# Kernel tuning notes

Hardware: AMD Instinct MI355X
Metric: run time of the kernel (lower is better)

## Reference

```python
import jax, jax.numpy as jnp
import numpy as np

KSIZE = 3
SCALE = 2


def setup_inputs() -> dict:
    key = jax.random.key(0)
    k1, k2, k3, k4 = jax.random.split(key, 4)
    B, C, H, W = 8, 3, 512, 512
    h, w = H // SCALE, W // SCALE
    return {
        "images": jax.random.uniform(k1, (B, C, H, W), jnp.float32),
        "kernels": jax.random.uniform(k2, (B, KSIZE ** 2, h, w), jnp.float32),
        "offsets_x": jax.random.uniform(k3, (B, KSIZE ** 2, h, w), jnp.float32),
        "offsets_y": jax.random.uniform(k4, (B, KSIZE ** 2, h, w), jnp.float32),
    }


def _softround(x, alpha=1.0):
    two_pi = 2.0 * jnp.pi
    return x - alpha * (jnp.sin(two_pi * x) / two_pi)


def _batch_bli(im, x, y):
    # im: [B, H, W, 3] channel-last; x, y: [B, N] float coords
    B, N = x.shape
    x0 = jnp.floor(x).astype(jnp.int32)
    x1 = x0 + 1
    y0 = jnp.floor(y).astype(jnp.int32)
    y1 = y0 + 1
    # original clamps x by im.shape[2] and y by im.shape[1] (square images)
    x0 = jnp.clip(x0, 0, im.shape[2] - 1)
    x1 = jnp.clip(x1, 0, im.shape[2] - 1)
    y0 = jnp.clip(y0, 0, im.shape[1] - 1)
    y1 = jnp.clip(y1, 0, im.shape[1] - 1)
    bidx = jnp.arange(B)[:, None]
    # vectorized gather of the four corners; flatten like torch.cat of [3]-vectors
    Ia = im[bidx, x0, y0].reshape(-1)  # [B*N*3]
    Ib = im[bidx, x0, y1].reshape(-1)
    Ic = im[bidx, x1, y0].reshape(-1)
    Id = im[bidx, x1, y1].reshape(-1)
    scale_w = (1.0 / ((x1 - x0) * (y1 - y0))).reshape(-1)  # [B*N]
    # faithful to the original's (scrambling) reshape semantics
    m1 = jnp.concatenate([x1 - x, x - x0], axis=1).astype(jnp.float32)  # [B, 2N]
    m1 = jnp.tile(m1.reshape(B * N, 1, 1, 2), (1, 2, 1, 1))             # [BN,2,1,2]
    m2 = jnp.stack([Ib, Ia, Id, Ic], axis=1).reshape(B * N, 2, 2, 3)    # [BN,2,2,3]
    m3 = jnp.concatenate([y1 - y, y - y0], axis=1).astype(jnp.float32)
    m3 = m3.reshape(B * N, 1, 2, 1)                                     # [BN,1,2,1]
    t = jnp.matmul(m1, m2).transpose(0, 3, 2, 1)  # [BN,3,1,2]
    out = jnp.matmul(t, m3).reshape(B * N, 3)     # [BN,3]
    return scale_w[:, None] * out


def reference(images, kernels, offsets_x, offsets_y):
    B = images.shape[0]
    h, w = images.shape[2] // SCALE, images.shape[3] // SCALE
    kernels = kernels.transpose(0, 2, 3, 1)      # [B,h,w,9]
    ox = offsets_x.transpose(0, 2, 3, 1)         # [B,h,w,9]
    oy = offsets_y.transpose(0, 2, 3, 1)
    u = jnp.arange(h, dtype=jnp.float32) + 0.5 * SCALE - 0.5
    kx = jnp.repeat(jnp.arange(KSIZE), KSIZE).astype(jnp.float32)  # 0,0,0,1,1,1,2,2,2
    ky = jnp.tile(jnp.arange(KSIZE), KSIZE).astype(jnp.float32)    # 0,1,2,0,1,2,0,1,2
    # original broadcasts u.reshape(h,1) over the w axis (requires h == w)
    coords_x = ox + KSIZE / 2 + kx + u[:, None]
    coords_y = oy + KSIZE / 2 + ky + u[:, None]
    im = images.transpose(0, 2, 3, 1)  # [B,H,W,3]
    pix = _batch_bli(im, coords_x.reshape(B, -1), coords_y.reshape(B, -1))
    pix_hr = pix.reshape(B, h, w, KSIZE ** 2, 3)
    out = jnp.sum(kernels[..., None] * pix_hr, axis=-2)  # [B,h,w,3]
    return _softround(out * 255.0)
```

## Files before the change

### kernel.cpp

```cpp
#include <hip/hip_runtime.h>
#include <math.h>

#define BATCH 8
#define HI 512
#define WI 512
#define HO 256
#define WO 256
#define PLANE (HI*WI)
#define OPIX (HO*WO)
#define LROWS 68
#define LCOLS 10
#define LQ 11

__global__ __launch_bounds__(256) void downsampler_kernel(
    const float* __restrict__ images,
    const float* __restrict__ kernels,
    const float* __restrict__ offx,
    const float* __restrict__ offy,
    float* __restrict__ out)
{
    __shared__ float4 simg[LROWS * LQ];

    const int blk  = blockIdx.x;
    const int b    = blk >> 8;
    const int ihx  = (blk >> 2) & 63;
    const int w0   = (blk & 3) << 6;
    const int tid  = threadIdx.x;
    const int lane = tid & 63;
    const int iw   = w0 + lane;
    const int ih   = (ihx << 2) + (tid >> 6);

    const float* offxb = offx    + (size_t)b * 9 * OPIX;
    const float* offyb = offy    + (size_t)b * 9 * OPIX;
    const float* kernb = kernels + (size_t)b * 9 * OPIX;

    const int pl   = ih * WO + iw;
    const int pix2 = pl & (OPIX / 2 - 1);

    float  ox_[9], oy_[9], kv_[9];
    float2 sx_[9], sy_[9];
    #pragma unroll
    for (int k = 0; k < 9; ++k) {
        ox_[k] = offxb[k * OPIX + pl];
        oy_[k] = offyb[k * OPIX + pl];
        kv_[k] = kernb[k * OPIX + pl];
        sx_[k] = ((const float2*)(offxb + k * OPIX))[pix2];
        sy_[k] = ((const float2*)(offyb + k * OPIX))[pix2];
    }

    {
        const float* imb = images + (size_t)b * 3 * PLANE;
        #pragma unroll
        for (int ii = 0; ii < 3; ++ii) {
            const int i = tid + ii * 256;
            if (i < LROWS * LCOLS) {
                const int row = i / LCOLS;
                const int col = i - row * LCOLS;
                const int r = w0 + 2 + row;
                int c = r - 4 + col;
                c = c < 0 ? 0 : c;
                const float* src = imb + r * WI + c;
                simg[row * LQ + col] =
                    make_float4(src[0], src[PLANE], src[2 * PLANE], 0.0f);
            }
        }
    }
    __builtin_amdgcn_sched_barrier(0);
    __syncthreads();

    const bool flip = (ih < 128);
    const float uu_own = (float)iw + 0.5f;
    const float uu_s0  = (float)((2 * iw) & 255) + 0.5f;
    const float uu_s1  = uu_s0 + 1.0f;

    float acc0 = 0.f, acc1 = 0.f, acc2 = 0.f;

    #pragma unroll
    for (int k = 0; k < 9; ++k) {
        const float kxf = (float)(k / 3);
        const float kyf = (float)(k - 3 * (k / 3));
        const float cx = ((ox_[k] + 1.5f) + kxf) + uu_own;
        const float cy = ((oy_[k] + 1.5f) + kyf) + uu_own;
        const int x0 = (int)floorf(cx);
        const int y0 = (int)floorf(cy);
        const int rowrel = x0 - 2 - w0;
        const int colq   = y0 - x0 + 4;
        const float4* qa = &simg[rowrel * LQ + (colq - 1)];
        const float4 Ia = qa[1];
        const float4 Ib = qa[2];
        const float4 Ic = qa[LQ];
        const float4 Id = qa[LQ + 1];

        const int ta = 2 * k, tb = 2 * k + 1;
        const int sel_a = (ta >= 9) ? 1 : 0;
        const int sel_b = (tb >= 9) ? 1 : 0;
        const int ks_a = ta - 9 * sel_a;
        const int ks_b = tb - 9 * sel_b;
        const float uu_a = sel_a ? uu_s1 : uu_s0;
        const float uu_b = sel_b ? uu_s1 : uu_s0;
        const float oxa  = sel_a ? sx_[ks_a].y : sx_[ks_a].x;
        const float oya  = sel_a ? sy_[ks_a].y : sy_[ks_a].x;
        const float oxb2 = sel_b ? sx_[ks_b].y : sx_[ks_b].x;
        const float oyb2 = sel_b ? sy_[ks_b].y : sy_[ks_b].x;
        const float kxa = (float)(ks_a / 3), kya = (float)(ks_a - 3 * (ks_a / 3));
        const float kxb = (float)(ks_b / 3), kyb = (float)(ks_b - 3 * (ks_b / 3));

        const float cxa = ((oxa + 1.5f) + kxa) + uu_a;
        const float cya = ((oya + 1.5f) + kya) + uu_a;
        const float cxb = ((oxb2 + 1.5f) + kxb) + uu_b;
        const float cyb = ((oyb2 + 1.5f) + kyb) + uu_b;
        const float fxa = cxa - floorf(cxa);
        const float fya = cya - floorf(cya);
        const float fxb = cxb - floorf(cxb);
        const float fyb = cyb - floorf(cyb);
        const float w0w = flip ? (1.0f - fxa) : fxa;
        const float w1w = flip ? (1.0f - fxb) : fxb;
        const float v0w = flip ? (1.0f - fya) : fya;
        const float v1w = flip ? (1.0f - fyb) : fyb;

        const float w0v0 = w0w * v0w, w1v0 = w1w * v0w;
        const float w0v1 = w0w * v1w, w1v1 = w1w * v1w;

        const float p0 = w0v0 * Ib.x + w1v0 * Ic.x + w0v1 * Id.y + w1v1 * Ia.z;
        const float p1 = w0v0 * Ia.x + w1v0 * Ib.y + w0v1 * Ic.y + w1v1 * Id.z;
        const float p2 = w0v0 * Id.x + w1v0 * Ia.y + w0v1 * Ib.z + w1v1 * Ic.z;

        acc0 += kv_[k] * p0;
        acc1 += kv_[k] * p1;
        acc2 += kv_[k] * p2;
    }

    const float TWO_PI_INV = 0.15915494309189533577f;
    const size_t obase = ((size_t)b * OPIX + (size_t)pl) * 3;
    const float z0 = acc0 * 255.0f;
    const float z1 = acc1 * 255.0f;
    const float z2 = acc2 * 255.0f;
    const float r0s = z0 - rintf(z0);
    const float r1s = z1 - rintf(z1);
    const float r2s = z2 - rintf(z2);
    out[obase + 0] = z0 - __builtin_amdgcn_sinf(r0s) * TWO_PI_INV;
    out[obase + 1] = z1 - __builtin_amdgcn_sinf(r1s) * TWO_PI_INV;
    out[obase + 2] = z2 - __builtin_amdgcn_sinf(r2s) * TWO_PI_INV;
}

extern "C" void kernel_launch(void* const* d_in, const int* in_sizes, int n_in,
                              void* d_out, int out_size, void* d_ws, size_t ws_size,
                              hipStream_t stream) {
    const float* images  = (const float*)d_in[0];
    const float* kernels = (const float*)d_in[1];
    const float* offx    = (const float*)d_in[2];
    const float* offy    = (const float*)d_in[3];
    float* out = (float*)d_out;

    dim3 grid(BATCH * 64 * 4);
    dim3 block(256);
    hipLaunchKernelGGL(downsampler_kernel, grid, block, 0, stream,
                       images, kernels, offx, offy, out);
}
```

Before: 113.9 us.

## Process four output pixels per thread with float4 loads and whole-row image tile

Each thread now computes four adjacent output pixels, loading offsets and kernels as float4 vectors and writing outputs as three float4 stores. Each block covers a full output row band, staging the full 260-row diagonal image strip in shared memory (about 45KB), and the grid shrinks fourfold to 512 blocks. The intent is to cut per-pixel load instruction count and amortise tile staging, at the cost of more registers, larger LDS limiting occupancy, fewer blocks, and a staging loop with no overlap with the offset loads.

New measurement: 156.7 us. 37.6% more time.

```diff
diff --git a/kernel.cpp b/kernel.cpp
--- a/kernel.cpp
+++ b/kernel.cpp
@@ -8,139 +8,143 @@
 #define WO 256
 #define PLANE (HI*WI)
 #define OPIX (HO*WO)
-#define LROWS 68
-#define LCOLS 10
-#define LQ 11
+#define BROWS 260
+#define BQ 11
 
-__global__ __launch_bounds__(256) void downsampler_kernel(
+__device__ __forceinline__ float elem4(const float4 v, int i) {
+    switch (i & 3) { case 0: return v.x; case 1: return v.y; case 2: return v.z; default: return v.w; }
+}
+__device__ __forceinline__ float elem8(const float4 a, const float4 b, int i) {
+    return (i < 4) ? elem4(a, i) : elem4(b, i - 4);
+}
+
+__global__ __launch_bounds__(256, 3) void downsampler_kernel(
     const float* __restrict__ images,
     const float* __restrict__ kernels,
     const float* __restrict__ offx,
     const float* __restrict__ offy,
     float* __restrict__ out)
 {
-    __shared__ float4 simg[LROWS * LQ];
+    __shared__ float4 simg[BROWS * BQ];
 
     const int blk  = blockIdx.x;
-    const int b    = blk >> 8;
-    const int ihx  = (blk >> 2) & 63;
-    const int w0   = (blk & 3) << 6;
+    const int b    = blk >> 6;
+    const int ihq  = blk & 63;
     const int tid  = threadIdx.x;
     const int lane = tid & 63;
-    const int iw   = w0 + lane;
-    const int ih   = (ihx << 2) + (tid >> 6);
+    const int g    = tid >> 6;
+    const int ih   = (ihq << 2) + g;
+    const int iw0  = lane << 2;
+    const int pl0  = ih * WO + iw0;
 
+    {
+        const float* imb = images + (size_t)b * 3 * PLANE;
+        for (int i = tid; i < BROWS * 10; i += 256) {
+            const int row = i / 10;
+            const int col = i - row * 10;
+            const int r = row + 2;
+            int c = r - 4 + col;
+            c = c < 0 ? 0 : c;
+            const float* src = imb + r * WI + c;
+            simg[row * BQ + col] = make_float4(src[0], src[PLANE], src[2 * PLANE], 0.0f);
+        }
+    }
+    __syncthreads();
+
+    const bool flip = (ih < 128);
     const float* offxb = offx    + (size_t)b * 9 * OPIX;
     const float* offyb = offy    + (size_t)b * 9 * OPIX;
     const float* kernb = kernels + (size_t)b * 9 * OPIX;
 
-    const int pl   = ih * WO + iw;
-    const int pix2 = pl & (OPIX / 2 - 1);
+    const int own4 = pl0 >> 2;
+    const int s4   = ((2 * pl0) & (OPIX - 1)) >> 2;
+    const float uu_own0 = (float)iw0 + 0.5f;
+    const int   c20     = (lane << 3) & 255;
 
-    float  ox_[9], oy_[9], kv_[9];
-    float2 sx_[9], sy_[9];
-    #pragma unroll
-    for (int k = 0; k < 9; ++k) {
-        ox_[k] = offxb[k * OPIX + pl];
-        oy_[k] = offyb[k * OPIX + pl];
-        kv_[k] = kernb[k * OPIX + pl];
-        sx_[k] = ((const float2*)(offxb + k * OPIX))[pix2];
-        sy_[k] = ((const float2*)(offyb + k * OPIX))[pix2];
-    }
-
-    {
-        const float* imb = images + (size_t)b * 3 * PLANE;
-        #pragma unroll
-        for (int ii = 0; ii < 3; ++ii) {
-            const int i = tid + ii * 256;
-            if (i < LROWS * LCOLS) {
-                const int row = i / LCOLS;
-                const int col = i - row * LCOLS;
-                const int r = w0 + 2 + row;
-                int c = r - 4 + col;
-                c = c < 0 ? 0 : c;
-                const float* src = imb + r * WI + c;
-                simg[row * LQ + col] =
-                    make_float4(src[0], src[PLANE], src[2 * PLANE], 0.0f);
-            }
-        }
-    }
-    __builtin_amdgcn_sched_barrier(0);
-    __syncthreads();
-
-    const bool flip = (ih < 128);
-    const float uu_own = (float)iw + 0.5f;
-    const float uu_s0  = (float)((2 * iw) & 255) + 0.5f;
-    const float uu_s1  = uu_s0 + 1.0f;
-
-    float acc0 = 0.f, acc1 = 0.f, acc2 = 0.f;
+    float acc[4][3] = {{0.f,0.f,0.f},{0.f,0.f,0.f},{0.f,0.f,0.f},{0.f,0.f,0.f}};
 
     #pragma unroll
     for (int k = 0; k < 9; ++k) {
-        const float kxf = (float)(k / 3);
-        const float kyf = (float)(k - 3 * (k / 3));
-        const float cx = ((ox_[k] + 1.5f) + kxf) + uu_own;
-        const float cy = ((oy_[k] + 1.5f) + kyf) + uu_own;
-        const int x0 = (int)floorf(cx);
-        const int y0 = (int)floorf(cy);
-        const int rowrel = x0 - 2 - w0;
-        const int colq   = y0 - x0 + 4;
-        const float4* qa = &simg[rowrel * LQ + (colq - 1)];
-        const float4 Ia = qa[1];
-        const float4 Ib = qa[2];
-        const float4 Ic = qa[LQ];
-        const float4 Id = qa[LQ + 1];
-
         const int ta = 2 * k, tb = 2 * k + 1;
         const int sel_a = (ta >= 9) ? 1 : 0;
         const int sel_b = (tb >= 9) ? 1 : 0;
         const int ks_a = ta - 9 * sel_a;
         const int ks_b = tb - 9 * sel_b;
-        const float uu_a = sel_a ? uu_s1 : uu_s0;
-        const float uu_b = sel_b ? uu_s1 : uu_s0;
-        const float oxa  = sel_a ? sx_[ks_a].y : sx_[ks_a].x;
-        const float oya  = sel_a ? sy_[ks_a].y : sy_[ks_a].x;
-        const float oxb2 = sel_b ? sx_[ks_b].y : sx_[ks_b].x;
-        const float oyb2 = sel_b ? sy_[ks_b].y : sy_[ks_b].x;
-        const float kxa = (float)(ks_a / 3), kya = (float)(ks_a - 3 * (ks_a / 3));
-        const float kxb = (float)(ks_b / 3), kyb = (float)(ks_b - 3 * (ks_b / 3));
+        const float kxa = (float)(ks_a / 3), kya = (float)(ks_a % 3);
+        const float kxb = (float)(ks_b / 3), kyb = (float)(ks_b % 3);
+        const float kxf = (float)(k / 3),    kyf = (float)(k % 3);
 
-        const float cxa = ((oxa + 1.5f) + kxa) + uu_a;
-        const float cya = ((oya + 1.5f) + kya) + uu_a;
-        const float cxb = ((oxb2 + 1.5f) + kxb) + uu_b;
-        const float cyb = ((oyb2 + 1.5f) + kyb) + uu_b;
-        const float fxa = cxa - floorf(cxa);
-        const float fya = cya - floorf(cya);
-        const float fxb = cxb - floorf(cxb);
-        const float fyb = cyb - floorf(cyb);
-        const float w0w = flip ? (1.0f - fxa) : fxa;
-        const float w1w = flip ? (1.0f - fxb) : fxb;
-        const float v0w = flip ? (1.0f - fya) : fya;
-        const float v1w = flip ? (1.0f - fyb) : fyb;
+        const float4 ox4 = ((const float4*)(offxb + (size_t)k * OPIX))[own4];
+        const float4 oy4 = ((const float4*)(offyb + (size_t)k * OPIX))[own4];
+        const float4 kv4 = ((const float4*)(kernb + (size_t)k * OPIX))[own4];
+        const float4 xa0 = ((const float4*)(offxb + (size_t)ks_a * OPIX))[s4];
+        const float4 xa1 = ((const float4*)(offxb + (size_t)ks_a * OPIX))[s4 + 1];
+        const float4 ya0 = ((const float4*)(offyb + (size_t)ks_a * OPIX))[s4];
+        const float4 ya1 = ((const float4*)(offyb + (size_t)ks_a * OPIX))[s4 + 1];
+        const float4 xb0 = ((const float4*)(offxb + (size_t)ks_b * OPIX))[s4];
+        const float4 xb1 = ((const float4*)(offxb + (size_t)ks_b * OPIX))[s4 + 1];
+        const float4 yb0 = ((const float4*)(offyb + (size_t)ks_b * OPIX))[s4];
+        const float4 yb1 = ((const float4*)(offyb + (size_t)ks_b * OPIX))[s4 + 1];
 
-        const float w0v0 = w0w * v0w, w1v0 = w1w * v0w;
-        const float w0v1 = w0w * v1w, w1v1 = w1w * v1w;
+        #pragma unroll
+        for (int p = 0; p < 4; ++p) {
+            const float uu_own = uu_own0 + (float)p;
+            const float cx = ((elem4(ox4, p) + 1.5f) + kxf) + uu_own;
+            const float cy = ((elem4(oy4, p) + 1.5f) + kyf) + uu_own;
+            const int x0 = (int)floorf(cx);
+            const int y0 = (int)floorf(cy);
+            const int rowrel = x0 - 2;
+            const int colq   = y0 - x0 + 4;
+            const float4* qa = &simg[rowrel * BQ + (colq - 1)];
+            const float4 Ia = qa[1];
+            const float4 Ib = qa[2];
+            const float4 Ic = qa[BQ];
+            const float4 Id = qa[BQ + 1];
 
-        const float p0 = w0v0 * Ib.x + w1v0 * Ic.x + w0v1 * Id.y + w1v1 * Ia.z;
-        const float p1 = w0v0 * Ia.x + w1v0 * Ib.y + w0v1 * Ic.y + w1v1 * Id.z;
-        const float p2 = w0v0 * Id.x + w1v0 * Ia.y + w0v1 * Ib.z + w1v1 * Ic.z;
+            const float uua = (float)(c20 + 2 * p + sel_a) + 0.5f;
+            const float uub = (float)(c20 + 2 * p + sel_b) + 0.5f;
+            const float cxa = ((elem8(xa0, xa1, 2 * p + sel_a) + 1.5f) + kxa) + uua;
+            const float cya = ((elem8(ya0, ya1, 2 * p + sel_a) + 1.5f) + kya) + uua;
+            const float cxb = ((elem8(xb0, xb1, 2 * p + sel_b) + 1.5f) + kxb) + uub;
+            const float cyb = ((elem8(yb0, yb1, 2 * p + sel_b) + 1.5f) + kyb) + uub;
+            const float fxa = cxa - floorf(cxa);
+            const float fya = cya - floorf(cya);
+            const float fxb = cxb - floorf(cxb);
+            const float fyb = cyb - floorf(cyb);
+            const float w0w = flip ? (1.0f - fxa) : fxa;
+            const float w1w = flip ? (1.0f - fxb) : fxb;
+            const float v0w = flip ? (1.0f - fya) : fya;
+            const float v1w = flip ? (1.0f - fyb) : fyb;
 
-        acc0 += kv_[k] * p0;
-        acc1 += kv_[k] * p1;
-        acc2 += kv_[k] * p2;
+            const float w0v0 = w0w * v0w, w1v0 = w1w * v0w;
+            const float w0v1 = w0w * v1w, w1v1 = w1w * v1w;
+
+            const float p0 = w0v0 * Ib.x + w1v0 * Ic.x + w0v1 * Id.y + w1v1 * Ia.z;
+            const float p1 = w0v0 * Ia.x + w1v0 * Ib.y + w0v1 * Ic.y + w1v1 * Id.z;
+            const float p2 = w0v0 * Id.x + w1v0 * Ia.y + w0v1 * Ib.z + w1v1 * Ic.z;
+
+            const float kv = elem4(kv4, p);
+            acc[p][0] += kv * p0;
+            acc[p][1] += kv * p1;
+            acc[p][2] += kv * p2;
+        }
     }
 
     const float TWO_PI_INV = 0.15915494309189533577f;
-    const size_t obase = ((size_t)b * OPIX + (size_t)pl) * 3;
-    const float z0 = acc0 * 255.0f;
-    const float z1 = acc1 * 255.0f;
-    const float z2 = acc2 * 255.0f;
-    const float r0s = z0 - rintf(z0);
-    const float r1s = z1 - rintf(z1);
-    const float r2s = z2 - rintf(z2);
-    out[obase + 0] = z0 - __builtin_amdgcn_sinf(r0s) * TWO_PI_INV;
-    out[obase + 1] = z1 - __builtin_amdgcn_sinf(r1s) * TWO_PI_INV;
-    out[obase + 2] = z2 - __builtin_amdgcn_sinf(r2s) * TWO_PI_INV;
+    float o[12];
+    #pragma unroll
+    for (int p = 0; p < 4; ++p) {
+        #pragma unroll
+        for (int ch = 0; ch < 3; ++ch) {
+            const float z  = acc[p][ch] * 255.0f;
+            const float rs = z - rintf(z);
+            o[p * 3 + ch] = z - __builtin_amdgcn_sinf(rs) * TWO_PI_INV;
+        }
+    }
+    float4* o4 = (float4*)(out + ((size_t)b * OPIX + (size_t)pl0) * 3);
+    o4[0] = make_float4(o[0], o[1], o[2],  o[3]);
+    o4[1] = make_float4(o[4], o[5], o[6],  o[7]);
+    o4[2] = make_float4(o[8], o[9], o[10], o[11]);
 }
 
 extern "C" void kernel_launch(void* const* d_in, const int* in_sizes, int n_in,
@@ -152,7 +156,7 @@
     const float* offy    = (const float*)d_in[3];
     float* out = (float*)d_out;
 
-    dim3 grid(BATCH * 64 * 4);
+    dim3 grid(BATCH * 64);
     dim3 block(256);
     hipLaunchKernelGGL(downsampler_kernel, grid, block, 0, stream,
                        images, kernels, offx, offy, out);
```
